# Performance work log

Hardware: AMD Instinct MI355X
Metric: run time of the kernel (lower is better)

## Reference

```python
import jax, jax.numpy as jnp
import numpy as np

MASK_FILL = -1e10
LOG_2PI = float(np.log(2.0 * np.pi))


def setup_inputs() -> dict:
    key = jax.random.key(0)
    k1, k2, k3 = jax.random.split(key, 3)
    bs, seq_len, emb_dim = 32, 512, 512
    T = 2048
    emb = jax.random.normal(k1, (bs, seq_len, emb_dim), dtype=jnp.float32)
    # positive durations; rescale so the max total duration over the batch == T exactly,
    # matching torch's T = sum(durations).int().max()
    d = jax.random.uniform(k2, (bs, seq_len), dtype=jnp.float32, minval=0.5, maxval=1.0)
    d = d * (T / jnp.max(jnp.sum(d, axis=1)))
    log_sigma = jax.random.normal(k3, (1,), dtype=jnp.float32) * 0.1
    return {"emb": emb, "durations": d, "log_sigma": log_sigma, "T": T}


def reference(emb, durations, log_sigma, T):
    # emb: (bs, S, E); durations: (bs, S); log_sigma: (1,); T: static int
    bs, S, E = emb.shape
    ls = log_sigma[0]
    sigma = jnp.exp(ls)
    # Gaussian centers per token: cumsum - 0.5*dur  -> (bs, S)
    centers = jnp.cumsum(durations, axis=1) - 0.5 * durations
    t = jnp.arange(T, dtype=emb.dtype)  # frame indices (T,)
    # Normal(loc=centers, scale=sigma).log_prob(t + 0.5)  -> (bs, T, S)
    z = (t[None, :, None] + 0.5 - centers[:, None, :]) / sigma
    logp = -0.5 * z * z - ls - 0.5 * LOG_2PI
    # mask out zero-duration tokens
    logp = jnp.where((durations == 0.0)[:, None, :], MASK_FILL, logp)
    w = jax.nn.softmax(logp, axis=2)  # (bs, T, S)
    x = jnp.einsum('bts,bse->bte', w, emb)  # (bs, T, E)
    total = jnp.sum(durations, axis=1)  # (bs,)
    out_mask = t[None, :] < total[:, None]  # (bs, T) bool
    return x, out_mask
```

## Files before the change

kernel.cpp:

```cpp
#include <hip/hip_runtime.h>
#include <math.h>

#define BS 32
#define S_TOK 512
#define E_DIM 512
#define T_FR 2048
#define FPB 16
#define WMAX 32
#define THRESH -25.0f


typedef float vfloat4 __attribute__((ext_vector_type(4)));

struct RowMeta { float m; float inv_l; int lo; int cnt; };

__global__ __launch_bounds__(64) void scan_kernel(
    const float* __restrict__ dur,
    float* __restrict__ centers,
    float* __restrict__ totals) {
  int b = blockIdx.x;
  int lane = threadIdx.x;
  const float* d = dur + b * S_TOK;
  int base = lane * 8;
  double local[8];
  double run = 0.0;
#pragma unroll
  for (int i = 0; i < 8; ++i) { run += (double)d[base + i]; local[i] = run; }
  double sum = run;
#pragma unroll
  for (int off = 1; off < 64; off <<= 1) {
    double v = __shfl_up(sum, off, 64);
    if (lane >= off) sum += v;
  }
  double excl = sum - run;
#pragma unroll
  for (int i = 0; i < 8; ++i) {
    centers[b * S_TOK + base + i] =
        (float)(excl + local[i] - 0.5 * (double)d[base + i]);
  }
  if (lane == 63) totals[b] = (float)sum;
}

__global__ __launch_bounds__(256) void meta_kernel(
    const float* __restrict__ centers,
    const float* __restrict__ log_sigma,
    RowMeta* __restrict__ meta) {
  int b = blockIdx.x >> 3;
  int t = ((blockIdx.x & 7) << 8) + threadIdx.x;

  __shared__ float cbS[S_TOK];
  for (int i = threadIdx.x; i < S_TOK; i += 256)
    cbS[i] = centers[b * S_TOK + i];
  __syncthreads();

  float inv_sigma = expf(-log_sigma[0]);
  float tq = (float)t + 0.5f;

  auto V = [&](int s) {
    float z = (tq - cbS[s]) * inv_sigma;
    return -0.5f * z * z;
  };

  int lo = 0, hi = S_TOK;
  while (lo < hi) {
    int mid = (lo + hi) >> 1;
    if (cbS[mid] < tq) lo = mid + 1; else hi = mid;
  }
  int best; float m;
  if (lo == 0) { best = 0; m = V(0); }
  else if (lo == S_TOK) { best = S_TOK - 1; m = V(best); }
  else {
    float va = V(lo - 1), vb = V(lo);
    if (va >= vb) { best = lo - 1; m = va; } else { best = lo; m = vb; }
  }

  int wl = best, wh = best;
  while (wl > 0 && V(wl - 1) > m + THRESH) --wl;
  while (wh < S_TOK - 1 && V(wh + 1) > m + THRESH) ++wh;

  float l = 0.0f;
  for (int s = wl; s <= wh; ++s) l += expf(V(s) - m);

  RowMeta mt;
  mt.m = m;
  mt.inv_l = 1.0f / l;
  mt.lo = wl;
  mt.cnt = wh - wl + 1;
  meta[b * T_FR + t] = mt;
}

__global__ __launch_bounds__(128) void fused_kernel(
    const float* __restrict__ emb,
    const float* __restrict__ centers,
    const float* __restrict__ log_sigma,
    const RowMeta* __restrict__ meta,
    const float* __restrict__ totals,
    float* __restrict__ x,
    float* __restrict__ mask_out) {
  int id = blockIdx.x;
  int sw = ((id & 7) << 9) + (id >> 3);
  int b = sw >> 7;
  int t0 = (sw & 127) << 4;

  int tid = threadIdx.x;

  __shared__ float wT[WMAX][FPB];
  __shared__ RowMeta metaS[FPB];

  if (tid < FPB) metaS[tid] = meta[b * T_FR + t0 + tid];
  __syncthreads();

  int ulo = metaS[0].lo, uhi = metaS[0].lo + metaS[0].cnt - 1;
#pragma unroll
  for (int f = 1; f < FPB; ++f) {
    ulo = min(ulo, metaS[f].lo);
    uhi = max(uhi, metaS[f].lo + metaS[f].cnt - 1);
  }
  int cnt = min(uhi - ulo + 1, WMAX);

  float inv_sigma = expf(-log_sigma[0]);
  const float* cb = centers + b * S_TOK;

  for (int k = tid; k < cnt * FPB; k += 128) {
    int i = k >> 4, f = k & 15;
    float c = cb[ulo + i];
    float tqf = (float)(t0 + f) + 0.5f;
    float z = (tqf - c) * inv_sigma;
    float v = -0.5f * z * z;
    float e = expf(v - metaS[f].m) * metaS[f].inv_l;
    wT[i][f] = (v - metaS[f].m > THRESH) ? e : 0.0f;
  }
  __syncthreads();

  const vfloat4* e4 =
      (const vfloat4*)emb + ((size_t)(b * S_TOK + ulo)) * (E_DIM / 4) + tid;
  vfloat4 acc[FPB];
#pragma unroll
  for (int f = 0; f < FPB; ++f) acc[f] = (vfloat4){0.f, 0.f, 0.f, 0.f};

  vfloat4 vcur = e4[0];
  for (int i = 0; i < cnt - 1; ++i) {
    vfloat4 vnext = e4[(size_t)(i + 1) * (E_DIM / 4)];
    const vfloat4* wp = (const vfloat4*)&wT[i][0];
    vfloat4 w0 = wp[0], w1 = wp[1], w2 = wp[2], w3 = wp[3];
    acc[0] += w0.x * vcur;  acc[1] += w0.y * vcur;
    acc[2] += w0.z * vcur;  acc[3] += w0.w * vcur;
    acc[4] += w1.x * vcur;  acc[5] += w1.y * vcur;
    acc[6] += w1.z * vcur;  acc[7] += w1.w * vcur;
    acc[8] += w2.x * vcur;  acc[9] += w2.y * vcur;
    acc[10] += w2.z * vcur; acc[11] += w2.w * vcur;
    acc[12] += w3.x * vcur; acc[13] += w3.y * vcur;
    acc[14] += w3.z * vcur; acc[15] += w3.w * vcur;
    vcur = vnext;
  }
  {
    const vfloat4* wp = (const vfloat4*)&wT[cnt - 1][0];
    vfloat4 w0 = wp[0], w1 = wp[1], w2 = wp[2], w3 = wp[3];
    acc[0] += w0.x * vcur;  acc[1] += w0.y * vcur;
    acc[2] += w0.z * vcur;  acc[3] += w0.w * vcur;
    acc[4] += w1.x * vcur;  acc[5] += w1.y * vcur;
    acc[6] += w1.z * vcur;  acc[7] += w1.w * vcur;
    acc[8] += w2.x * vcur;  acc[9] += w2.y * vcur;
    acc[10] += w2.z * vcur; acc[11] += w2.w * vcur;
    acc[12] += w3.x * vcur; acc[13] += w3.y * vcur;
    acc[14] += w3.z * vcur; acc[15] += w3.w * vcur;
  }

  vfloat4* xp = (vfloat4*)x + ((size_t)(b * T_FR + t0)) * (E_DIM / 4) + tid;
#pragma unroll
  for (int f = 0; f < FPB; ++f)
    xp[f * (E_DIM / 4)] = acc[f];

  if (tid < FPB) {
    int t = t0 + tid;
    mask_out[b * T_FR + t] = ((float)t < totals[b]) ? 1.0f : 0.0f;
  }
}

extern "C" void kernel_launch(void* const* d_in, const int* in_sizes, int n_in,
                              void* d_out, int out_size, void* d_ws,
                              size_t ws_size, hipStream_t stream) {
  const float* emb = (const float*)d_in[0];
  const float* dur = (const float*)d_in[1];
  const float* log_sigma = (const float*)d_in[2];

  float* x = (float*)d_out;
  float* mask_out = x + (size_t)BS * T_FR * E_DIM;

  float* centers = (float*)d_ws;
  float* totals = centers + BS * S_TOK;
  RowMeta* meta = (RowMeta*)(totals + 64);

  scan_kernel<<<BS, 64, 0, stream>>>(dur, centers, totals);
  meta_kernel<<<BS * 8, 256, 0, stream>>>(centers, log_sigma, meta);
  fused_kernel<<<(BS * T_FR) / FPB, 128, 0, stream>>>(
      emb, centers, log_sigma, meta, totals, x, mask_out);
}
```

Before: 172.4 us.

## Process 32 frames per block with two half-blocks sharing the token window

```diff
diff --git a/kernel.cpp b/kernel.cpp
--- a/kernel.cpp
+++ b/kernel.cpp
@@ -5,8 +5,8 @@
 #define S_TOK 512
 #define E_DIM 512
 #define T_FR 2048
-#define FPB 16
-#define WMAX 32
+#define FPB 32
+#define WMAX 36
 #define THRESH -25.0f
 
 
@@ -89,7 +89,7 @@
   meta[b * T_FR + t] = mt;
 }
 
-__global__ __launch_bounds__(128) void fused_kernel(
+__global__ __launch_bounds__(256) void fused_kernel(
     const float* __restrict__ emb,
     const float* __restrict__ centers,
     const float* __restrict__ log_sigma,
@@ -98,11 +98,13 @@
     float* __restrict__ x,
     float* __restrict__ mask_out) {
   int id = blockIdx.x;
-  int sw = ((id & 7) << 9) + (id >> 3);
-  int b = sw >> 7;
-  int t0 = (sw & 127) << 4;
+  int sw = ((id & 7) << 8) + (id >> 3);
+  int b = sw >> 6;
+  int t0 = (sw & 63) << 5;
 
   int tid = threadIdx.x;
+  int half = tid >> 7;
+  int lane = tid & 127;
 
   __shared__ float wT[WMAX][FPB];
   __shared__ RowMeta metaS[FPB];
@@ -121,8 +123,8 @@
   float inv_sigma = expf(-log_sigma[0]);
   const float* cb = centers + b * S_TOK;
 
-  for (int k = tid; k < cnt * FPB; k += 128) {
-    int i = k >> 4, f = k & 15;
+  for (int k = tid; k < cnt * FPB; k += 256) {
+    int i = k >> 5, f = k & 31;
     float c = cb[ulo + i];
     float tqf = (float)(t0 + f) + 0.5f;
     float z = (tqf - c) * inv_sigma;
@@ -133,15 +135,16 @@
   __syncthreads();
 
   const vfloat4* e4 =
-      (const vfloat4*)emb + ((size_t)(b * S_TOK + ulo)) * (E_DIM / 4) + tid;
-  vfloat4 acc[FPB];
+      (const vfloat4*)emb + ((size_t)(b * S_TOK + ulo)) * (E_DIM / 4) + lane;
+  vfloat4 acc[16];
 #pragma unroll
-  for (int f = 0; f < FPB; ++f) acc[f] = (vfloat4){0.f, 0.f, 0.f, 0.f};
+  for (int f = 0; f < 16; ++f) acc[f] = (vfloat4){0.f, 0.f, 0.f, 0.f};
 
   vfloat4 vcur = e4[0];
-  for (int i = 0; i < cnt - 1; ++i) {
-    vfloat4 vnext = e4[(size_t)(i + 1) * (E_DIM / 4)];
-    const vfloat4* wp = (const vfloat4*)&wT[i][0];
+  vfloat4 vnext = e4[(size_t)min(1, cnt - 1) * (E_DIM / 4)];
+  for (int i = 0; i < cnt; ++i) {
+    vfloat4 vfut = e4[(size_t)min(i + 2, cnt - 1) * (E_DIM / 4)];
+    const vfloat4* wp = (const vfloat4*)&wT[i][half << 4];
     vfloat4 w0 = wp[0], w1 = wp[1], w2 = wp[2], w3 = wp[3];
     acc[0] += w0.x * vcur;  acc[1] += w0.y * vcur;
     acc[2] += w0.z * vcur;  acc[3] += w0.w * vcur;
@@ -151,25 +154,14 @@
     acc[10] += w2.z * vcur; acc[11] += w2.w * vcur;
     acc[12] += w3.x * vcur; acc[13] += w3.y * vcur;
     acc[14] += w3.z * vcur; acc[15] += w3.w * vcur;
-    vcur = vnext;
-  }
-  {
-    const vfloat4* wp = (const vfloat4*)&wT[cnt - 1][0];
-    vfloat4 w0 = wp[0], w1 = wp[1], w2 = wp[2], w3 = wp[3];
-    acc[0] += w0.x * vcur;  acc[1] += w0.y * vcur;
-    acc[2] += w0.z * vcur;  acc[3] += w0.w * vcur;
-    acc[4] += w1.x * vcur;  acc[5] += w1.y * vcur;
-    acc[6] += w1.z * vcur;  acc[7] += w1.w * vcur;
-    acc[8] += w2.x * vcur;  acc[9] += w2.y * vcur;
-    acc[10] += w2.z * vcur; acc[11] += w2.w * vcur;
-    acc[12] += w3.x * vcur; acc[13] += w3.y * vcur;
-    acc[14] += w3.z * vcur; acc[15] += w3.w * vcur;
+    vcur = vnext; vnext = vfut;
   }
 
-  vfloat4* xp = (vfloat4*)x + ((size_t)(b * T_FR + t0)) * (E_DIM / 4) + tid;
+  vfloat4* xp = (vfloat4*)x +
+      ((size_t)(b * T_FR + t0 + (half << 4))) * (E_DIM / 4) + lane;
 #pragma unroll
-  for (int f = 0; f < FPB; ++f)
-    xp[f * (E_DIM / 4)] = acc[f];
+  for (int f = 0; f < 16; ++f)
+    xp[(size_t)f * (E_DIM / 4)] = acc[f];
 
   if (tid < FPB) {
     int t = t0 + tid;
@@ -193,6 +185,6 @@
 
   scan_kernel<<<BS, 64, 0, stream>>>(dur, centers, totals);
   meta_kernel<<<BS * 8, 256, 0, stream>>>(centers, log_sigma, meta);
-  fused_kernel<<<(BS * T_FR) / FPB, 128, 0, stream>>>(
+  fused_kernel<<<(BS * T_FR) / FPB, 256, 0, stream>>>(
       emb, centers, log_sigma, meta, totals, x, mask_out);
 }
```

Result: no change. 174.9 us (+1.5%).
